# Kernel tuning notes

Hardware: AMD Instinct MI355X
Metric: run time of the kernel (lower is better)

The kernel has to match this reference:

```python
import jax, jax.numpy as jnp
import numpy as np

B, T, D = 8, 2048, 1024  # batch, block_size (== seq len), n_embd


def setup_inputs() -> dict:
    key = jax.random.key(0)
    k1, k2 = jax.random.split(key)
    x = jax.random.normal(k1, (B, T, D), dtype=jnp.float32)
    W_qkv = jax.random.normal(k2, (3 * D, D), dtype=jnp.float32) * 0.02
    b_qkv = jnp.zeros((3 * D,), dtype=jnp.float32)
    ln_w = jnp.ones((D,), dtype=jnp.float32)
    ln_b = jnp.zeros((D,), dtype=jnp.float32)
    return {"x": x, "W_qkv": W_qkv, "b_qkv": b_qkv, "ln_w": ln_w, "ln_b": ln_b}


def reference(x, W_qkv, b_qkv, ln_w, ln_b):
    # qkv projection: Linear(n_embd, 3*n_embd)
    qkv = jnp.einsum('btd,ed->bte', x, W_qkv) + b_qkv  # [B,T,3D]
    q, k, v = jnp.split(qkv, 3, axis=-1)
    # causal linear attention (no softmax)
    scale = np.sqrt(D * T).astype(np.float32)
    scores = jnp.einsum('bid,bjd->bij', q, k) / scale  # [B,T,T]
    mask = jnp.tril(jnp.ones((T, T), dtype=scores.dtype))
    scores = scores * mask
    y = jnp.einsum('bij,bjd->bid', scores, v)  # [B,T,D]
    # LayerNorm over last dim, eps=1e-5
    mu = jnp.mean(y, axis=-1, keepdims=True)
    var = jnp.mean(jnp.square(y - mu), axis=-1, keepdims=True)
    y_hat = (y - mu) * jax.lax.rsqrt(var + 1e-5)
    return y_hat * ln_w + ln_b
```

## Files before the change

### kernel.cpp

```cpp
#include <hip/hip_runtime.h>
#include <hip/hip_bf16.h>
#include <stdint.h>

typedef __attribute__((ext_vector_type(8))) short bf16x8;
typedef __attribute__((ext_vector_type(4))) float f32x4;
typedef __attribute__((ext_vector_type(4))) unsigned short us4;

__device__ __forceinline__ unsigned short f2b(float f) {
  union { float f; unsigned u; } u;
  u.f = f;
  unsigned r = u.u + 0x7fffu + ((u.u >> 16) & 1u);
  return (unsigned short)(r >> 16);
}

__device__ __forceinline__ void gload_lds16(const void* g, void* lds) {
  __builtin_amdgcn_global_load_lds(
      (const __attribute__((address_space(1))) unsigned int*)(uintptr_t)g,
      (__attribute__((address_space(3))) unsigned int*)(uintptr_t)lds,
      16, 0, 0);
}

#define TILE_M 128
#define TILE_K 32

__device__ __forceinline__ void stage_tile(const unsigned short* __restrict__ g,
                                           long ld, long row0,
                                           unsigned short* lds, int tid) {
  int w = tid >> 6, lane = tid & 63;
#pragma unroll
  for (int j = 0; j < 2; ++j) {
    int o = ((w * 2 + j) << 10) + lane * 16;
    int row = o >> 6;
    int col = (o & 63) >> 1;
    const unsigned short* gp = g + (row0 + row) * ld + col;
    gload_lds16(gp, (char*)lds + ((w * 2 + j) << 10));
  }
}

__global__ __launch_bounds__(256, 2) void gemm1_qkv(
    const unsigned short* __restrict__ A,
    const unsigned short* __restrict__ Bm,
    const float* __restrict__ bias,
    unsigned short* __restrict__ qb, unsigned short* __restrict__ kb,
    unsigned short* __restrict__ vb) {
  __shared__ unsigned short lsA[TILE_M * TILE_K];
  __shared__ unsigned short lsB[TILE_M * TILE_K];
  int tid = threadIdx.x;
  int lane = tid & 63, w = tid >> 6;
  int wr = w >> 1, wc = w & 1;
  long bm0 = (long)blockIdx.y * TILE_M;
  long bn0 = (long)blockIdx.x * TILE_M;
  f32x4 acc[4][4] = {};
  int r = lane & 15, g = lane >> 4;
  for (int kt = 0; kt < 1024 / TILE_K; ++kt) {
    long k0 = (long)kt * TILE_K;
    stage_tile(A + k0, 1024, bm0, lsA, tid);
    stage_tile(Bm + k0, 1024, bn0, lsB, tid);
    __syncthreads();
    bf16x8 aF[4], bF[4];
#pragma unroll
    for (int m = 0; m < 4; ++m)
      aF[m] = *(const bf16x8*)(lsA + (wr * 64 + m * 16 + r) * 32 + g * 8);
#pragma unroll
    for (int n = 0; n < 4; ++n)
      bF[n] = *(const bf16x8*)(lsB + (wc * 64 + n * 16 + r) * 32 + g * 8);
#pragma unroll
    for (int m = 0; m < 4; ++m)
#pragma unroll
      for (int n = 0; n < 4; ++n)
        acc[m][n] = __builtin_amdgcn_mfma_f32_16x16x32_bf16(aF[m], bF[n], acc[m][n], 0, 0, 0);
    __syncthreads();
  }
  int part = blockIdx.x >> 3;
  unsigned short* O = (part == 0) ? qb : (part == 1) ? kb : vb;
  long cl0 = (long)(blockIdx.x & 7) * 128;
#pragma unroll
  for (int n = 0; n < 4; ++n) {
    long cc = wc * 64 + n * 16 + r;
    float bv = bias[bn0 + cc];
#pragma unroll
    for (int m = 0; m < 4; ++m)
#pragma unroll
      for (int j = 0; j < 4; ++j) {
        long row = bm0 + wr * 64 + m * 16 + g * 4 + j;
        O[row * 1024 + cl0 + cc] = f2b(acc[m][n][j] + bv);
      }
  }
}

__global__ __launch_bounds__(256, 2) void gemm2_scores(
    const unsigned short* __restrict__ qm, const unsigned short* __restrict__ km,
    unsigned short* __restrict__ scores, float inv_scale) {
  __shared__ unsigned short lsA[TILE_M * TILE_K];
  __shared__ unsigned short lsB[TILE_M * TILE_K];
  int p = 135 - blockIdx.x;
  int bi = 0, base = 0;
  while (p >= base + bi + 1) { base += bi + 1; ++bi; }
  int bj = p - base;
  int b = blockIdx.y;
  int tid = threadIdx.x;
  int lane = tid & 63, w = tid >> 6;
  int wr = w >> 1, wc = w & 1;
  long bm0 = (long)bi * TILE_M;
  long bn0 = (long)bj * TILE_M;
  const unsigned short* A = qm + (long)b * 2048 * 1024;
  const unsigned short* Bm = km + (long)b * 2048 * 1024;
  f32x4 acc[4][4] = {};
  int r = lane & 15, g = lane >> 4;
  for (int kt = 0; kt < 1024 / TILE_K; ++kt) {
    long k0 = (long)kt * TILE_K;
    stage_tile(A + k0, 1024, bm0, lsA, tid);
    stage_tile(Bm + k0, 1024, bn0, lsB, tid);
    __syncthreads();
    bf16x8 aF[4], bF[4];
#pragma unroll
    for (int m = 0; m < 4; ++m)
      aF[m] = *(const bf16x8*)(lsA + (wr * 64 + m * 16 + r) * 32 + g * 8);
#pragma unroll
    for (int n = 0; n < 4; ++n)
      bF[n] = *(const bf16x8*)(lsB + (wc * 64 + n * 16 + r) * 32 + g * 8);
#pragma unroll
    for (int m = 0; m < 4; ++m)
#pragma unroll
      for (int n = 0; n < 4; ++n)
        acc[m][n] = __builtin_amdgcn_mfma_f32_16x16x32_bf16(aF[m], bF[n], acc[m][n], 0, 0, 0);
    __syncthreads();
  }
  unsigned short* S = scores + (long)b * 2048 * 2048;
#pragma unroll
  for (int n = 0; n < 4; ++n) {
    long col = bn0 + wc * 64 + n * 16 + r;
#pragma unroll
    for (int m = 0; m < 4; ++m)
#pragma unroll
      for (int j = 0; j < 4; ++j) {
        long row = bm0 + wr * 64 + m * 16 + g * 4 + j;
        float v = acc[m][n][j] * inv_scale;
        if (col > row) v = 0.0f;
        S[row * 2048 + col] = f2b(v);
      }
  }
}

__global__ __launch_bounds__(256, 2) void gemm3_y(
    const unsigned short* __restrict__ scores, const unsigned short* __restrict__ vT,
    float* __restrict__ out) {
  __shared__ unsigned short lsA[TILE_M * TILE_K];
  __shared__ unsigned short lsB[TILE_M * TILE_K];
  int bn = blockIdx.x, bi = 15 - blockIdx.y, b = blockIdx.z;
  int tid = threadIdx.x;
  int lane = tid & 63, w = tid >> 6;
  int wr = w >> 1, wc = w & 1;
  long bm0 = (long)bi * TILE_M;
  long bn0 = (long)bn * TILE_M;
  const unsigned short* A = scores + (long)b * 2048 * 2048;
  const unsigned short* Bm = vT + (long)b * 1024 * 2048;
  f32x4 acc[4][4] = {};
  int r = lane & 15, g = lane >> 4;
  int KT = (bi + 1) * (TILE_M / TILE_K);
  for (int kt = 0; kt < KT; ++kt) {
    long k0 = (long)kt * TILE_K;
    stage_tile(A + k0, 2048, bm0, lsA, tid);
    stage_tile(Bm + k0, 2048, bn0, lsB, tid);
    __syncthreads();
    bf16x8 aF[4], bF[4];
#pragma unroll
    for (int m = 0; m < 4; ++m)
      aF[m] = *(const bf16x8*)(lsA + (wr * 64 + m * 16 + r) * 32 + g * 8);
#pragma unroll
    for (int n = 0; n < 4; ++n)
      bF[n] = *(const bf16x8*)(lsB + (wc * 64 + n * 16 + r) * 32 + g * 8);
#pragma unroll
    for (int m = 0; m < 4; ++m)
#pragma unroll
      for (int n = 0; n < 4; ++n)
        acc[m][n] = __builtin_amdgcn_mfma_f32_16x16x32_bf16(aF[m], bF[n], acc[m][n], 0, 0, 0);
    __syncthreads();
  }
#pragma unroll
  for (int n = 0; n < 4; ++n) {
    long col = bn0 + wc * 64 + n * 16 + r;
#pragma unroll
    for (int m = 0; m < 4; ++m)
#pragma unroll
      for (int j = 0; j < 4; ++j) {
        long row = bm0 + wr * 64 + m * 16 + g * 4 + j;
        out[((long)b * 2048 + row) * 1024 + col] = acc[m][n][j];
      }
  }
}

__global__ void cvt_f32_bf16(const float* __restrict__ in,
                             unsigned short* __restrict__ out, long n) {
  long i = ((long)blockIdx.x * blockDim.x + threadIdx.x) * 8;
  if (i + 8 > n) return;
  float4 a = *(const float4*)(in + i);
  float4 b = *(const float4*)(in + i + 4);
  bf16x8 o;
  o[0] = (short)f2b(a.x); o[1] = (short)f2b(a.y);
  o[2] = (short)f2b(a.z); o[3] = (short)f2b(a.w);
  o[4] = (short)f2b(b.x); o[5] = (short)f2b(b.y);
  o[6] = (short)f2b(b.z); o[7] = (short)f2b(b.w);
  *(bf16x8*)(out + i) = o;
}

__global__ void transpose_v(const unsigned short* __restrict__ vm,
                            unsigned short* __restrict__ vT) {
  __shared__ unsigned short tile[64][72];
  int t0 = blockIdx.x * 64, d0 = blockIdx.y * 64, b = blockIdx.z;
  int tid = threadIdx.x;
  int sub = tid & 15, grp = tid >> 4;
#pragma unroll
  for (int it = 0; it < 4; ++it) {
    int tt = it * 16 + grp;
    int dd = sub * 4;
    const unsigned short* src =
        vm + ((long)(b * 2048 + t0 + tt)) * 1024 + d0 + dd;
    *(us4*)&tile[tt][dd] = *(const us4*)src;
  }
  __syncthreads();
#pragma unroll
  for (int it = 0; it < 4; ++it) {
    int dd = it * 16 + grp;
    int ts = sub * 4;
    us4 o;
    o[0] = tile[ts + 0][dd];
    o[1] = tile[ts + 1][dd];
    o[2] = tile[ts + 2][dd];
    o[3] = tile[ts + 3][dd];
    *(us4*)(vT + ((long)b * 1024 + d0 + dd) * 2048 + t0 + ts) = o;
  }
}

__global__ void ln_kernel(float* __restrict__ y, const float* __restrict__ wv,
                          const float* __restrict__ bv) {
  __shared__ float sm[4];
  long row = blockIdx.x;
  int tid = threadIdx.x;
  float4 v = *(const float4*)(y + row * 1024 + tid * 4);
  float s = v.x + v.y + v.z + v.w;
#pragma unroll
  for (int o = 32; o > 0; o >>= 1) s += __shfl_xor(s, o, 64);
  if ((tid & 63) == 0) sm[tid >> 6] = s;
  __syncthreads();
  float mu = (sm[0] + sm[1] + sm[2] + sm[3]) * (1.0f / 1024.0f);
  float dx = v.x - mu, dy = v.y - mu, dz = v.z - mu, dw = v.w - mu;
  float sq = dx * dx + dy * dy + dz * dz + dw * dw;
#pragma unroll
  for (int o = 32; o > 0; o >>= 1) sq += __shfl_xor(sq, o, 64);
  __syncthreads();
  if ((tid & 63) == 0) sm[tid >> 6] = sq;
  __syncthreads();
  float var = (sm[0] + sm[1] + sm[2] + sm[3]) * (1.0f / 1024.0f);
  float inv = rsqrtf(var + 1e-5f);
  float4 w4 = *(const float4*)(wv + tid * 4);
  float4 b4 = *(const float4*)(bv + tid * 4);
  float4 o4;
  o4.x = dx * inv * w4.x + b4.x;
  o4.y = dy * inv * w4.y + b4.y;
  o4.z = dz * inv * w4.z + b4.z;
  o4.w = dw * inv * w4.w + b4.w;
  *(float4*)(y + row * 1024 + tid * 4) = o4;
}

extern "C" void kernel_launch(void* const* d_in, const int* in_sizes, int n_in,
                              void* d_out, int out_size, void* d_ws, size_t ws_size,
                              hipStream_t stream) {
  const float* x = (const float*)d_in[0];
  const float* W = (const float*)d_in[1];
  const float* bq = (const float*)d_in[2];
  const float* lnw = (const float*)d_in[3];
  const float* lnb = (const float*)d_in[4];
  float* out = (float*)d_out;

  char* ws = (char*)d_ws;
  unsigned short* qb = (unsigned short*)(ws);
  unsigned short* kb = (unsigned short*)(ws + 33554432L);
  unsigned short* vb = (unsigned short*)(ws + 67108864L);
  unsigned short* vT = (unsigned short*)(ws + 100663296L);
  unsigned short* xb = (unsigned short*)(ws + 134217728L);
  unsigned short* Wb = (unsigned short*)(ws + 167772160L);
  unsigned short* sc = (unsigned short*)(ws + 134217728L);

  const float inv_scale = 1.0f / sqrtf(1024.0f * 2048.0f);

  cvt_f32_bf16<<<8192, 256, 0, stream>>>(x, xb, 16384L * 1024);
  cvt_f32_bf16<<<1536, 256, 0, stream>>>(W, Wb, 3072L * 1024);
  gemm1_qkv<<<dim3(24, 128), 256, 0, stream>>>(xb, Wb, bq, qb, kb, vb);
  transpose_v<<<dim3(32, 16, 8), 256, 0, stream>>>(vb, vT);
  gemm2_scores<<<dim3(136, 8), 256, 0, stream>>>(qb, kb, sc, inv_scale);
  gemm3_y<<<dim3(8, 16, 8), 256, 0, stream>>>(sc, vT, out);
  ln_kernel<<<16384, 256, 0, stream>>>(out, lnw, lnb);
}
```

Baseline: 448.6 us.

## Fuse V transpose into QKV GEMM epilogue, merge converts, deepen K step

The QKV GEMM epilogue now writes the V part directly in transposed layout, which removes the separate transpose kernel and one round trip of V through memory. The two fp32-to-bf16 conversion launches are merged into one. All three GEMMs now stage two 32-wide K slices per barrier pair, which halves the number of __syncthreads and doubles LDS use per block. The transposed V stores are 8-byte scattered writes with a 4 KB stride, which may coalesce poorly.

```diff
diff --git a/kernel.cpp b/kernel.cpp
--- a/kernel.cpp
+++ b/kernel.cpp
@@ -37,14 +37,32 @@
   }
 }
 
+__device__ __forceinline__ void mfma_step(const unsigned short* lsA,
+                                          const unsigned short* lsB,
+                                          int wr, int wc, int r, int g,
+                                          f32x4 (&acc)[4][4]) {
+  bf16x8 aF[4], bF[4];
+#pragma unroll
+  for (int m = 0; m < 4; ++m)
+    aF[m] = *(const bf16x8*)(lsA + (wr * 64 + m * 16 + r) * 32 + g * 8);
+#pragma unroll
+  for (int n = 0; n < 4; ++n)
+    bF[n] = *(const bf16x8*)(lsB + (wc * 64 + n * 16 + r) * 32 + g * 8);
+#pragma unroll
+  for (int m = 0; m < 4; ++m)
+#pragma unroll
+    for (int n = 0; n < 4; ++n)
+      acc[m][n] = __builtin_amdgcn_mfma_f32_16x16x32_bf16(aF[m], bF[n], acc[m][n], 0, 0, 0);
+}
+
 __global__ __launch_bounds__(256, 2) void gemm1_qkv(
     const unsigned short* __restrict__ A,
     const unsigned short* __restrict__ Bm,
     const float* __restrict__ bias,
     unsigned short* __restrict__ qb, unsigned short* __restrict__ kb,
-    unsigned short* __restrict__ vb) {
-  __shared__ unsigned short lsA[TILE_M * TILE_K];
-  __shared__ unsigned short lsB[TILE_M * TILE_K];
+    unsigned short* __restrict__ vT) {
+  __shared__ unsigned short lsA[2][TILE_M * TILE_K];
+  __shared__ unsigned short lsB[2][TILE_M * TILE_K];
   int tid = threadIdx.x;
   int lane = tid & 63, w = tid >> 6;
   int wr = w >> 1, wc = w & 1;
@@ -52,47 +70,60 @@
   long bn0 = (long)blockIdx.x * TILE_M;
   f32x4 acc[4][4] = {};
   int r = lane & 15, g = lane >> 4;
-  for (int kt = 0; kt < 1024 / TILE_K; ++kt) {
-    long k0 = (long)kt * TILE_K;
-    stage_tile(A + k0, 1024, bm0, lsA, tid);
-    stage_tile(Bm + k0, 1024, bn0, lsB, tid);
-    __syncthreads();
-    bf16x8 aF[4], bF[4];
-#pragma unroll
-    for (int m = 0; m < 4; ++m)
-      aF[m] = *(const bf16x8*)(lsA + (wr * 64 + m * 16 + r) * 32 + g * 8);
-#pragma unroll
-    for (int n = 0; n < 4; ++n)
-      bF[n] = *(const bf16x8*)(lsB + (wc * 64 + n * 16 + r) * 32 + g * 8);
-#pragma unroll
-    for (int m = 0; m < 4; ++m)
-#pragma unroll
-      for (int n = 0; n < 4; ++n)
-        acc[m][n] = __builtin_amdgcn_mfma_f32_16x16x32_bf16(aF[m], bF[n], acc[m][n], 0, 0, 0);
+  for (int kt = 0; kt < 1024 / 64; ++kt) {
+    long k0 = (long)kt * 64;
+    stage_tile(A + k0, 1024, bm0, lsA[0], tid);
+    stage_tile(A + k0 + 32, 1024, bm0, lsA[1], tid);
+    stage_tile(Bm + k0, 1024, bn0, lsB[0], tid);
+    stage_tile(Bm + k0 + 32, 1024, bn0, lsB[1], tid);
+    __syncthreads();
+    mfma_step(lsA[0], lsB[0], wr, wc, r, g, acc);
+    mfma_step(lsA[1], lsB[1], wr, wc, r, g, acc);
     __syncthreads();
   }
   int part = blockIdx.x >> 3;
-  unsigned short* O = (part == 0) ? qb : (part == 1) ? kb : vb;
   long cl0 = (long)(blockIdx.x & 7) * 128;
-#pragma unroll
-  for (int n = 0; n < 4; ++n) {
-    long cc = wc * 64 + n * 16 + r;
-    float bv = bias[bn0 + cc];
-#pragma unroll
-    for (int m = 0; m < 4; ++m)
-#pragma unroll
-      for (int j = 0; j < 4; ++j) {
-        long row = bm0 + wr * 64 + m * 16 + g * 4 + j;
-        O[row * 1024 + cl0 + cc] = f2b(acc[m][n][j] + bv);
+  if (part < 2) {
+    unsigned short* O = (part == 0) ? qb : kb;
+#pragma unroll
+    for (int n = 0; n < 4; ++n) {
+      long cc = wc * 64 + n * 16 + r;
+      float bv = bias[bn0 + cc];
+#pragma unroll
+      for (int m = 0; m < 4; ++m)
+#pragma unroll
+        for (int j = 0; j < 4; ++j) {
+          long row = bm0 + wr * 64 + m * 16 + g * 4 + j;
+          O[row * 1024 + cl0 + cc] = f2b(acc[m][n][j] + bv);
+        }
+    }
+  } else {
+    long bq = bm0 >> 11;
+    long tbase = bm0 & 2047;
+#pragma unroll
+    for (int n = 0; n < 4; ++n) {
+      long cc = wc * 64 + n * 16 + r;
+      float bv = bias[bn0 + cc];
+      long d = cl0 + cc;
+#pragma unroll
+      for (int m = 0; m < 4; ++m) {
+        long t = tbase + wr * 64 + m * 16 + g * 4;
+        us4 o;
+        o[0] = f2b(acc[m][n][0] + bv);
+        o[1] = f2b(acc[m][n][1] + bv);
+        o[2] = f2b(acc[m][n][2] + bv);
+        o[3] = f2b(acc[m][n][3] + bv);
+        *(us4*)(vT + bq * 2097152 + d * 2048 + t) = o;
       }
+    }
   }
 }
 
 __global__ __launch_bounds__(256, 2) void gemm2_scores(
     const unsigned short* __restrict__ qm, const unsigned short* __restrict__ km,
     unsigned short* __restrict__ scores, float inv_scale) {
-  __shared__ unsigned short lsA[TILE_M * TILE_K];
-  __shared__ unsigned short lsB[TILE_M * TILE_K];
+  __shared__ unsigned short lsA[2][TILE_M * TILE_K];
+  __shared__ unsigned short lsB[2][TILE_M * TILE_K];
   int p = 135 - blockIdx.x;
   int bi = 0, base = 0;
   while (p >= base + bi + 1) { base += bi + 1; ++bi; }
@@ -107,23 +138,15 @@
   const unsigned short* Bm = km + (long)b * 2048 * 1024;
   f32x4 acc[4][4] = {};
   int r = lane & 15, g = lane >> 4;
-  for (int kt = 0; kt < 1024 / TILE_K; ++kt) {
-    long k0 = (long)kt * TILE_K;
-    stage_tile(A + k0, 1024, bm0, lsA, tid);
-    stage_tile(Bm + k0, 1024, bn0, lsB, tid);
-    __syncthreads();
-    bf16x8 aF[4], bF[4];
-#pragma unroll
-    for (int m = 0; m < 4; ++m)
-      aF[m] = *(const bf16x8*)(lsA + (wr * 64 + m * 16 + r) * 32 + g * 8);
-#pragma unroll
-    for (int n = 0; n < 4; ++n)
-      bF[n] = *(const bf16x8*)(lsB + (wc * 64 + n * 16 + r) * 32 + g * 8);
-#pragma unroll
-    for (int m = 0; m < 4; ++m)
-#pragma unroll
-      for (int n = 0; n < 4; ++n)
-        acc[m][n] = __builtin_amdgcn_mfma_f32_16x16x32_bf16(aF[m], bF[n], acc[m][n], 0, 0, 0);
+  for (int kt = 0; kt < 1024 / 64; ++kt) {
+    long k0 = (long)kt * 64;
+    stage_tile(A + k0, 1024, bm0, lsA[0], tid);
+    stage_tile(A + k0 + 32, 1024, bm0, lsA[1], tid);
+    stage_tile(Bm + k0, 1024, bn0, lsB[0], tid);
+    stage_tile(Bm + k0 + 32, 1024, bn0, lsB[1], tid);
+    __syncthreads();
+    mfma_step(lsA[0], lsB[0], wr, wc, r, g, acc);
+    mfma_step(lsA[1], lsB[1], wr, wc, r, g, acc);
     __syncthreads();
   }
   unsigned short* S = scores + (long)b * 2048 * 2048;
@@ -145,8 +168,8 @@
 __global__ __launch_bounds__(256, 2) void gemm3_y(
     const unsigned short* __restrict__ scores, const unsigned short* __restrict__ vT,
     float* __restrict__ out) {
-  __shared__ unsigned short lsA[TILE_M * TILE_K];
-  __shared__ unsigned short lsB[TILE_M * TILE_K];
+  __shared__ unsigned short lsA[2][TILE_M * TILE_K];
+  __shared__ unsigned short lsB[2][TILE_M * TILE_K];
   int bn = blockIdx.x, bi = 15 - blockIdx.y, b = blockIdx.z;
   int tid = threadIdx.x;
   int lane = tid & 63, w = tid >> 6;
@@ -157,24 +180,16 @@
   const unsigned short* Bm = vT + (long)b * 1024 * 2048;
   f32x4 acc[4][4] = {};
   int r = lane & 15, g = lane >> 4;
-  int KT = (bi + 1) * (TILE_M / TILE_K);
-  for (int kt = 0; kt < KT; ++kt) {
-    long k0 = (long)kt * TILE_K;
-    stage_tile(A + k0, 2048, bm0, lsA, tid);
-    stage_tile(Bm + k0, 2048, bn0, lsB, tid);
-    __syncthreads();
-    bf16x8 aF[4], bF[4];
-#pragma unroll
-    for (int m = 0; m < 4; ++m)
-      aF[m] = *(const bf16x8*)(lsA + (wr * 64 + m * 16 + r) * 32 + g * 8);
-#pragma unroll
-    for (int n = 0; n < 4; ++n)
-      bF[n] = *(const bf16x8*)(lsB + (wc * 64 + n * 16 + r) * 32 + g * 8);
-#pragma unroll
-    for (int m = 0; m < 4; ++m)
-#pragma unroll
-      for (int n = 0; n < 4; ++n)
-        acc[m][n] = __builtin_amdgcn_mfma_f32_16x16x32_bf16(aF[m], bF[n], acc[m][n], 0, 0, 0);
+  int KT2 = (bi + 1) * 2;
+  for (int kt = 0; kt < KT2; ++kt) {
+    long k0 = (long)kt * 64;
+    stage_tile(A + k0, 2048, bm0, lsA[0], tid);
+    stage_tile(A + k0 + 32, 2048, bm0, lsA[1], tid);
+    stage_tile(Bm + k0, 2048, bn0, lsB[0], tid);
+    stage_tile(Bm + k0 + 32, 2048, bn0, lsB[1], tid);
+    __syncthreads();
+    mfma_step(lsA[0], lsB[0], wr, wc, r, g, acc);
+    mfma_step(lsA[1], lsB[1], wr, wc, r, g, acc);
     __syncthreads();
   }
 #pragma unroll
@@ -190,46 +205,27 @@
   }
 }
 
-__global__ void cvt_f32_bf16(const float* __restrict__ in,
-                             unsigned short* __restrict__ out, long n) {
+__global__ void cvt_f32_bf16(const float* __restrict__ x, unsigned short* __restrict__ xb,
+                             const float* __restrict__ W, unsigned short* __restrict__ Wb) {
+  const long n1 = 16384L * 1024;
+  const long n2 = 3072L * 1024;
   long i = ((long)blockIdx.x * blockDim.x + threadIdx.x) * 8;
-  if (i + 8 > n) return;
-  float4 a = *(const float4*)(in + i);
-  float4 b = *(const float4*)(in + i + 4);
+  const float* in;
+  unsigned short* out;
+  if (i < n1) { in = x + i; out = xb + i; }
+  else {
+    long k = i - n1;
+    if (k >= n2) return;
+    in = W + k; out = Wb + k;
+  }
+  float4 a = *(const float4*)(in);
+  float4 b = *(const float4*)(in + 4);
   bf16x8 o;
   o[0] = (short)f2b(a.x); o[1] = (short)f2b(a.y);
   o[2] = (short)f2b(a.z); o[3] = (short)f2b(a.w);
   o[4] = (short)f2b(b.x); o[5] = (short)f2b(b.y);
   o[6] = (short)f2b(b.z); o[7] = (short)f2b(b.w);
-  *(bf16x8*)(out + i) = o;
-}
-
-__global__ void transpose_v(const unsigned short* __restrict__ vm,
-                            unsigned short* __restrict__ vT) {
-  __shared__ unsigned short tile[64][72];
-  int t0 = blockIdx.x * 64, d0 = blockIdx.y * 64, b = blockIdx.z;
-  int tid = threadIdx.x;
-  int sub = tid & 15, grp = tid >> 4;
-#pragma unroll
-  for (int it = 0; it < 4; ++it) {
-    int tt = it * 16 + grp;
-    int dd = sub * 4;
-    const unsigned short* src =
-        vm + ((long)(b * 2048 + t0 + tt)) * 1024 + d0 + dd;
-    *(us4*)&tile[tt][dd] = *(const us4*)src;
-  }
-  __syncthreads();
-#pragma unroll
-  for (int it = 0; it < 4; ++it) {
-    int dd = it * 16 + grp;
-    int ts = sub * 4;
-    us4 o;
-    o[0] = tile[ts + 0][dd];
-    o[1] = tile[ts + 1][dd];
-    o[2] = tile[ts + 2][dd];
-    o[3] = tile[ts + 3][dd];
-    *(us4*)(vT + ((long)b * 1024 + d0 + dd) * 2048 + t0 + ts) = o;
-  }
+  *(bf16x8*)(out) = o;
 }
 
 __global__ void ln_kernel(float* __restrict__ y, const float* __restrict__ wv,
@@ -276,7 +272,6 @@
   char* ws = (char*)d_ws;
   unsigned short* qb = (unsigned short*)(ws);
   unsigned short* kb = (unsigned short*)(ws + 33554432L);
-  unsigned short* vb = (unsigned short*)(ws + 67108864L);
   unsigned short* vT = (unsigned short*)(ws + 100663296L);
   unsigned short* xb = (unsigned short*)(ws + 134217728L);
   unsigned short* Wb = (unsigned short*)(ws + 167772160L);
@@ -284,10 +279,8 @@
 
   const float inv_scale = 1.0f / sqrtf(1024.0f * 2048.0f);
 
-  cvt_f32_bf16<<<8192, 256, 0, stream>>>(x, xb, 16384L * 1024);
-  cvt_f32_bf16<<<1536, 256, 0, stream>>>(W, Wb, 3072L * 1024);
-  gemm1_qkv<<<dim3(24, 128), 256, 0, stream>>>(xb, Wb, bq, qb, kb, vb);
-  transpose_v<<<dim3(32, 16, 8), 256, 0, stream>>>(vb, vT);
+  cvt_f32_bf16<<<9728, 256, 0, stream>>>(x, xb, W, Wb);
+  gemm1_qkv<<<dim3(24, 128), 256, 0, stream>>>(xb, Wb, bq, qb, kb, vT);
   gemm2_scores<<<dim3(136, 8), 256, 0, stream>>>(qb, kb, sc, inv_scale);
   gemm3_y<<<dim3(8, 16, 8), 256, 0, stream>>>(sc, vT, out);
   ln_kernel<<<16384, 256, 0, stream>>>(out, lnw, lnb);
```

Measured after the change: 397.0 us. 1.13x faster.
